# Performance work log

Measured on AMD Instinct MI355X. Metric: run time of the kernel, lower is better.

Reference implementation:

```python
import jax, jax.numpy as jnp
import numpy as np

NEG = -1e9


def _lstm_step(x, h, c, W_ih, W_hh, b_ih, b_hh):
    # torch LSTM gate order: i, f, g, o
    gates = x @ W_ih.T + b_ih + h @ W_hh.T + b_hh
    i, f, g, o = jnp.split(gates, 4, axis=-1)
    c_new = jax.nn.sigmoid(f) * c + jax.nn.sigmoid(i) * jnp.tanh(g)
    h_new = jax.nn.sigmoid(o) * jnp.tanh(c_new)
    return h_new, c_new


def _forward(encoder_states, emb, W_ih, W_hh, b_ih, b_hh, W_att,
             pad_mask, pointer_mask, token_ids, target_sequence,
             sos_token, eos_token, output_len):
    B, N, D = encoder_states.shape
    V = emb.shape[0]
    dt = encoder_states.dtype
    padf = pad_mask.astype(dt)
    enc = encoder_states * padf[..., None]          # zero padded node states
    # _init_lstm_state: mean of encoder states over valid nodes (pad-only mask)
    h0 = enc.sum(axis=1) / padf.sum(axis=1, keepdims=True)  # [B, D]
    # attention mask after pointer restriction: only valid leaf pointer nodes
    attn_mask = jnp.where(pointer_mask, jnp.asarray(0.0, dt), jnp.asarray(NEG, dt))
    n_ptr = pointer_mask.sum(axis=1).astype(dt)     # [B]
    thr = 1.0 / n_ptr                               # _threshold_cf = 1.0
    b_idx = jnp.arange(B)

    # teacher forcing: step 1 uses SOS, step s>1 uses target_sequence[s-1]
    sos_row = jnp.full((1, B), sos_token, dtype=target_sequence.dtype)
    inputs = jnp.concatenate([sos_row, target_sequence[1:output_len - 1]], axis=0)  # [T-1, B]

    def step(carry, inp):
        h, c = carry
        x = emb[inp]                                     # [B, E]
        h, c = _lstm_step(x, h, c, W_ih, W_hh, b_ih, b_hh)
        # Luong attention -> probabilities over tree nodes
        scores = jnp.einsum('bnd,bd->bn', enc, h @ W_att.T) + attn_mask
        probs = jax.nn.softmax(scores, axis=1)           # [B, N]
        # threshold: probabilities below 1/n_ptr are zeroed; only pointer nodes kept
        probs = jnp.where(pointer_mask & (probs >= thr[:, None]), probs, jnp.asarray(0.0, dt))
        # scatter(reduce='sum') node probabilities into vocab-sized output
        out = jnp.zeros((B, V), dt).at[b_idx[:, None], token_ids].add(probs)
        out = out.at[:, eos_token].set(1.0 - probs.sum(axis=1))
        return (h, c), out

    (_, _), outs = jax.lax.scan(step, (h0, h0), inputs)   # [T-1, B, V]
    out0 = jnp.zeros((B, V), dt).at[:, sos_token].set(1.0)
    return jnp.concatenate([out0[None], outs], axis=0)    # [T, B, V]


def setup_inputs() -> dict:
    key = jax.random.key(0)
    ks = jax.random.split(key, 10)
    B, N, D, E, V, T = 32, 2048, 512, 512, 32000, 32
    encoder_states = jax.random.normal(ks[0], (B, N, D), dtype=jnp.float32)
    lengths = jax.random.randint(ks[1], (B,), N // 2, N + 1)
    pad_mask = jnp.arange(N)[None, :] < lengths[:, None]            # [B, N] ragged trees
    leaf = jax.random.bernoulli(ks[2], 0.5, (B, N))
    pointer_mask = pad_mask & leaf                                  # valid leaf pointer nodes
    token_ids = jax.random.randint(ks[3], (B, N), 0, V, dtype=jnp.int32)
    target_sequence = jax.random.randint(ks[4], (T, B), 3, V, dtype=jnp.int32)
    s = 0.02
    emb = jax.random.normal(ks[5], (V, E), dtype=jnp.float32) * s
    W_ih = jax.random.normal(ks[6], (4 * D, E), dtype=jnp.float32) * s
    W_hh = jax.random.normal(ks[7], (4 * D, D), dtype=jnp.float32) * s
    b_ih = jnp.zeros((4 * D,), dtype=jnp.float32)
    b_hh = jnp.zeros((4 * D,), dtype=jnp.float32)
    W_att = jax.random.normal(ks[8], (D, D), dtype=jnp.float32) * s
    return {
        'encoder_states': encoder_states, 'emb': emb,
        'W_ih': W_ih, 'W_hh': W_hh, 'b_ih': b_ih, 'b_hh': b_hh, 'W_att': W_att,
        'pad_mask': pad_mask, 'pointer_mask': pointer_mask,
        'token_ids': token_ids, 'target_sequence': target_sequence,
        'sos_token': 1, 'eos_token': 2, 'output_len': T,
    }


def reference(encoder_states, emb, W_ih, W_hh, b_ih, b_hh, W_att,
              pad_mask, pointer_mask, token_ids, target_sequence,
              sos_token, eos_token, output_len):
    return _forward(encoder_states, emb, W_ih, W_hh, b_ih, b_hh, W_att,
                    pad_mask, pointer_mask, token_ids, target_sequence,
                    sos_token, eos_token, output_len)
```

## Files before the change

### kernel.cpp

```cpp
#include <hip/hip_runtime.h>
#include <math.h>

#define BB 32
#define NN 2048
#define DD 512
#define VV 32000
#define NSTEP 31

__device__ inline float sigm(float x){ return 1.0f/(1.0f+expf(-x)); }
__device__ inline float dot4(float4 a, float4 b){
  return a.x*b.x + a.y*b.y + a.z*b.z + a.w*b.w;
}

__device__ inline float red8(float a0,float a1,float a2,float a3,
                             float a4,float a5,float a6,float a7,int lane){
  float m01 = ((lane&1)? a1:a0) + __shfl_xor(((lane&1)? a0:a1),1,64);
  float m23 = ((lane&1)? a3:a2) + __shfl_xor(((lane&1)? a2:a3),1,64);
  float m45 = ((lane&1)? a5:a4) + __shfl_xor(((lane&1)? a4:a5),1,64);
  float m67 = ((lane&1)? a7:a6) + __shfl_xor(((lane&1)? a6:a7),1,64);
  float m03 = ((lane&2)? m23:m01) + __shfl_xor(((lane&2)? m01:m23),2,64);
  float m47 = ((lane&2)? m67:m45) + __shfl_xor(((lane&2)? m45:m67),2,64);
  float m   = ((lane&4)? m47:m03) + __shfl_xor(((lane&4)? m03:m47),4,64);
  m += __shfl_xor(m,8,64); m += __shfl_xor(m,16,64); m += __shfl_xor(m,32,64);
  return m;
}

__global__ __launch_bounds__(256) void k_cnt(
    const int* __restrict__ pad, const int* __restrict__ pmask,
    const int* __restrict__ sosp,
    float* __restrict__ cntp, float* __restrict__ thr, float* __restrict__ out,
    unsigned int* __restrict__ flags) {
  __shared__ int r1[256], r2[256];
  int b = blockIdx.x, tid = threadIdx.x;
  if (b == 0) {
    if (tid < 256)
      __hip_atomic_store(&flags[tid], 0u, __ATOMIC_RELAXED,
                         __HIP_MEMORY_SCOPE_AGENT);
    if (tid == 0)
      __hip_atomic_store(&flags[256], 0u, __ATOMIC_RELAXED,
                         __HIP_MEMORY_SCOPE_AGENT);
  }
  float4* orow4 = (float4*)(out + (size_t)b*VV);
  float4 z = {0.f,0.f,0.f,0.f};
  for (int i = tid; i < VV/4; i += 256) orow4[i] = z;
  int cp = 0, cq = 0;
  for (int n = tid; n < NN; n += 256) { cp += pad[b*NN+n]; cq += pmask[b*NN+n]; }
  r1[tid] = cp; r2[tid] = cq; __syncthreads();
  for (int st = 128; st; st >>= 1) {
    if (tid < st) { r1[tid] += r1[tid+st]; r2[tid] += r2[tid+st]; }
    __syncthreads();
  }
  if (tid == 0) {
    cntp[b] = (float)r1[0];
    thr[b]  = 1.0f/(float)r2[0];
    out[(size_t)b*VV + sosp[0]] = 1.0f;
  }
}

__global__ __launch_bounds__(128) void k_meanpart(
    const float* __restrict__ enc, const int* __restrict__ pad,
    float* __restrict__ hpart) {
  int b = blockIdx.x, ch = blockIdx.y, kq = threadIdx.x;
  int n0 = ch*32;
  float4 acc = {0.f,0.f,0.f,0.f};
#pragma unroll 8
  for (int r = 0; r < 32; r++) {
    int n = n0 + r;
    float msk = (float)pad[b*NN + n];
    float4 v = *(const float4*)(enc + ((size_t)(b*NN + n))*DD + kq*4);
    acc.x += msk*v.x; acc.y += msk*v.y; acc.z += msk*v.z; acc.w += msk*v.w;
  }
  *(float4*)(hpart + ((size_t)(b*64 + ch))*DD + kq*4) = acc;
}

__global__ __launch_bounds__(128) void k_meanfin(
    const float* __restrict__ hpart, const float* __restrict__ cntp,
    float* __restrict__ h0, float* __restrict__ c) {
  int b = blockIdx.x, kq = threadIdx.x;
  float4 acc = {0.f,0.f,0.f,0.f};
  for (int ch = 0; ch < 64; ch++) {
    float4 v = *(const float4*)(hpart + ((size_t)(b*64 + ch))*DD + kq*4);
    acc.x += v.x; acc.y += v.y; acc.z += v.z; acc.w += v.w;
  }
  float ic = 1.0f/cntp[b];
  acc.x *= ic; acc.y *= ic; acc.z *= ic; acc.w *= ic;
  *(float4*)(h0 + b*DD + kq*4) = acc;
  *(float4*)(c  + b*DD + kq*4) = acc;
}

__global__ __launch_bounds__(512, 2) void k_hloop(
    const float* __restrict__ h0, const float* __restrict__ Whh,
    const float* __restrict__ Wih, const float* __restrict__ bih,
    const float* __restrict__ bhh, const float* __restrict__ emb,
    const int* __restrict__ target, const int* __restrict__ sosp,
    float* __restrict__ H, unsigned int* __restrict__ flags) {
  __shared__ float spad[20736];
  float* g   = spad;
  float* Gls = spad + 256;
  int bi = blockIdx.x, d0 = bi*2;
  int tid = threadIdx.x;
  int w = tid>>6, lane = tid&63;
  float4 W0[8], W1[8], Wi0[8], Wi1[8];
#pragma unroll
  for (int j = 0; j < 8; j++) {
    int r = (j>>1)*DD + d0 + (j&1);
    const float* wp = Whh + (size_t)r*DD + lane*4;
    W0[j]  = *(const float4*)wp; W1[j]  = *(const float4*)(wp + 256);
    const float* ip = Wih + (size_t)r*DD + lane*4;
    Wi0[j] = *(const float4*)ip; Wi1[j] = *(const float4*)(ip + 256);
  }
  int jrole = lane & 7;
  int brow = (jrole>>1)*DD + d0 + (jrole&1);
  float biasj = bih[brow] + bhh[brow];
  int pb = tid>>1, pdd = tid&1;
  float creg = 0.f;
  if (tid < 64) creg = h0[pb*DD + d0 + pdd];

  {
    int sos = sosp[0];
    const float* xp = emb + (size_t)sos*DD + lane*4;
    float4 x0 = *(const float4*)xp, x1 = *(const float4*)(xp + 256);
    float a0 = dot4(x0,Wi0[0]) + dot4(x1,Wi1[0]);
    float a1 = dot4(x0,Wi0[1]) + dot4(x1,Wi1[1]);
    float a2 = dot4(x0,Wi0[2]) + dot4(x1,Wi1[2]);
    float a3 = dot4(x0,Wi0[3]) + dot4(x1,Wi1[3]);
    float a4 = dot4(x0,Wi0[4]) + dot4(x1,Wi1[4]);
    float a5 = dot4(x0,Wi0[5]) + dot4(x1,Wi1[5]);
    float a6 = dot4(x0,Wi0[6]) + dot4(x1,Wi1[6]);
    float a7 = dot4(x0,Wi0[7]) + dot4(x1,Wi1[7]);
    float v = red8(a0,a1,a2,a3,a4,a5,a6,a7,lane);
    if (lane < 8) {
      float vb = v + biasj;
#pragma unroll
      for (int bb = 0; bb < 4; bb++) Gls[(w*4+bb)*8 + lane] = vb;
    }
  }
  __syncthreads();

  for (int s = 0; s < NSTEP; s++) {
#pragma unroll
    for (int j = 0; j < 8; j++) {
      asm volatile("" : "+v"(W0[j].x), "+v"(W0[j].y),
                        "+v"(W0[j].z), "+v"(W0[j].w),
                        "+v"(W1[j].x), "+v"(W1[j].y),
                        "+v"(W1[j].z), "+v"(W1[j].w));
      asm volatile("" : "+v"(Wi0[j].x), "+v"(Wi0[j].y),
                        "+v"(Wi0[j].z), "+v"(Wi0[j].w),
                        "+v"(Wi1[j].x), "+v"(Wi1[j].y),
                        "+v"(Wi1[j].z), "+v"(Wi1[j].w));
    }
    const float* hin = (s == 0) ? h0 : (H + (size_t)(s-1)*BB*DD);
#pragma unroll
    for (int bb = 0; bb < 4; bb++) {
      int b = w*4 + bb;
      const float* hp = hin + b*DD + lane*4;
      float4 h0v = *(const float4*)hp, h1v = *(const float4*)(hp + 256);
      float a0 = dot4(h0v,W0[0]) + dot4(h1v,W1[0]);
      float a1 = dot4(h0v,W0[1]) + dot4(h1v,W1[1]);
      float a2 = dot4(h0v,W0[2]) + dot4(h1v,W1[2]);
      float a3 = dot4(h0v,W0[3]) + dot4(h1v,W1[3]);
      float a4 = dot4(h0v,W0[4]) + dot4(h1v,W1[4]);
      float a5 = dot4(h0v,W0[5]) + dot4(h1v,W1[5]);
      float a6 = dot4(h0v,W0[6]) + dot4(h1v,W1[6]);
      float a7 = dot4(h0v,W0[7]) + dot4(h1v,W1[7]);
      float v = red8(a0,a1,a2,a3,a4,a5,a6,a7,lane);
      if (lane < 8) g[b*8 + lane] = v;
    }
    float4 xg0[4], xg1[4];
    if (s < NSTEP-1) {
#pragma unroll
      for (int bb = 0; bb < 4; bb++) {
        int tg = target[(s+1)*BB + w*4 + bb];
        const float* xp = emb + (size_t)tg*DD + lane*4;
        xg0[bb] = *(const float4*)xp; xg1[bb] = *(const float4*)(xp + 256);
      }
    }
    __syncthreads();
    if (tid < 64) {
      const float* Gs = Gls + (s&1)*256;
      float gi = g[pb*8 + 0 + pdd] + Gs[pb*8 + 0 + pdd];
      float gf = g[pb*8 + 2 + pdd] + Gs[pb*8 + 2 + pdd];
      float gg = g[pb*8 + 4 + pdd] + Gs[pb*8 + 4 + pdd];
      float go = g[pb*8 + 6 + pdd] + Gs[pb*8 + 6 + pdd];
      creg = sigm(gf)*creg + sigm(gi)*tanhf(gg);
      float hn = sigm(go)*tanhf(creg);
      __hip_atomic_store(H + (size_t)s*BB*DD + pb*DD + d0 + pdd, hn,
                         __ATOMIC_RELAXED, __HIP_MEMORY_SCOPE_AGENT);
    }
    if (s == NSTEP-1) break;
    __syncthreads();
    unsigned tgt = (unsigned)(s+1);
    if (tid == 0)
      __hip_atomic_store(&flags[bi], tgt,
                         __ATOMIC_RELAXED, __HIP_MEMORY_SCOPE_AGENT);
    {
      float* Gd = Gls + ((s+1)&1)*256;
#pragma unroll
      for (int bb = 0; bb < 4; bb++) {
        float a0 = dot4(xg0[bb],Wi0[0]) + dot4(xg1[bb],Wi1[0]);
        float a1 = dot4(xg0[bb],Wi0[1]) + dot4(xg1[bb],Wi1[1]);
        float a2 = dot4(xg0[bb],Wi0[2]) + dot4(xg1[bb],Wi1[2]);
        float a3 = dot4(xg0[bb],Wi0[3]) + dot4(xg1[bb],Wi1[3]);
        float a4 = dot4(xg0[bb],Wi0[4]) + dot4(xg1[bb],Wi1[4]);
        float a5 = dot4(xg0[bb],Wi0[5]) + dot4(xg1[bb],Wi1[5]);
        float a6 = dot4(xg0[bb],Wi0[6]) + dot4(xg1[bb],Wi1[6]);
        float a7 = dot4(xg0[bb],Wi0[7]) + dot4(xg1[bb],Wi1[7]);
        float v = red8(a0,a1,a2,a3,a4,a5,a6,a7,lane);
        if (lane < 8) Gd[(w*4+bb)*8 + lane] = v + biasj;
      }
    }
    if (bi == 0 && tid < 64) {
      const unsigned int* fp = flags + tid*4;
      for (;;) {
        unsigned f0 = __hip_atomic_load(fp+0, __ATOMIC_RELAXED,
                                        __HIP_MEMORY_SCOPE_AGENT);
        unsigned f1 = __hip_atomic_load(fp+1, __ATOMIC_RELAXED,
                                        __HIP_MEMORY_SCOPE_AGENT);
        unsigned f2 = __hip_atomic_load(fp+2, __ATOMIC_RELAXED,
                                        __HIP_MEMORY_SCOPE_AGENT);
        unsigned f3 = __hip_atomic_load(fp+3, __ATOMIC_RELAXED,
                                        __HIP_MEMORY_SCOPE_AGENT);
        if (f0 >= tgt && f1 >= tgt && f2 >= tgt && f3 >= tgt) break;
        __builtin_amdgcn_s_sleep(1);
      }
      if (tid == 0)
        __hip_atomic_store(&flags[256], tgt,
                           __ATOMIC_RELAXED, __HIP_MEMORY_SCOPE_AGENT);
    }
    if (tid == 0) {
      while (__hip_atomic_load(&flags[256], __ATOMIC_RELAXED,
                               __HIP_MEMORY_SCOPE_AGENT) < tgt)
        __builtin_amdgcn_s_sleep(1);
    }
    __syncthreads();
  }
}

__global__ __launch_bounds__(256) void k_qallw(
    const float* __restrict__ H, const float* __restrict__ Watt,
    float* __restrict__ Q) {
  int nt = blockIdx.x, mg = blockIdx.y;
  int w = threadIdx.x>>6, lane = threadIdx.x&63;
  int m0 = mg*32 + w*8;
  float4 x0[8], x1[8];
#pragma unroll
  for (int j = 0; j < 8; j++) {
    const float* xp = H + (size_t)(m0 + j)*DD + lane*4;
    x0[j] = *(const float4*)xp; x1[j] = *(const float4*)(xp + 256);
  }
  int r0 = nt*16;
#pragma unroll 2
  for (int i = 0; i < 16; i++) {
    int r = r0 + i;
    const float* wp = Watt + (size_t)r*DD + lane*4;
    float4 w0 = *(const float4*)wp, w1 = *(const float4*)(wp + 256);
    float a0 = dot4(w0,x0[0]) + dot4(w1,x1[0]);
    float a1 = dot4(w0,x0[1]) + dot4(w1,x1[1]);
    float a2 = dot4(w0,x0[2]) + dot4(w1,x1[2]);
    float a3 = dot4(w0,x0[3]) + dot4(w1,x1[3]);
    float a4 = dot4(w0,x0[4]) + dot4(w1,x1[4]);
    float a5 = dot4(w0,x0[5]) + dot4(w1,x1[5]);
    float a6 = dot4(w0,x0[6]) + dot4(w1,x1[6]);
    float a7 = dot4(w0,x0[7]) + dot4(w1,x1[7]);
    float v = red8(a0,a1,a2,a3,a4,a5,a6,a7,lane);
    if (lane < 8) Q[(size_t)(m0 + lane)*DD + r] = v;
  }
}

__global__ __launch_bounds__(256) void k_scores3(
    const float* __restrict__ enc, const float* __restrict__ Q,
    float* __restrict__ S) {
  int nt = blockIdx.x, b = blockIdx.y;
  int w = threadIdx.x>>6, lane = threadIdx.x&63;
  int s0 = w*8;
  float4 q0[8], q1[8];
#pragma unroll
  for (int j = 0; j < 8; j++) {
    const float* qp = Q + (size_t)((s0 + j)*BB + b)*DD + lane*4;
    q0[j] = *(const float4*)qp; q1[j] = *(const float4*)(qp + 256);
  }
  int n0 = nt*32;
  int sl = s0 + (lane & 7);
#pragma unroll 2
  for (int i = 0; i < 32; i++) {
    int n = n0 + i;
    const float* ep = enc + ((size_t)(b*NN + n))*DD + lane*4;
    float4 e0 = *(const float4*)ep, e1 = *(const float4*)(ep + 256);
    float a0 = dot4(e0,q0[0]) + dot4(e1,q1[0]);
    float a1 = dot4(e0,q0[1]) + dot4(e1,q1[1]);
    float a2 = dot4(e0,q0[2]) + dot4(e1,q1[2]);
    float a3 = dot4(e0,q0[3]) + dot4(e1,q1[3]);
    float a4 = dot4(e0,q0[4]) + dot4(e1,q1[4]);
    float a5 = dot4(e0,q0[5]) + dot4(e1,q1[5]);
    float a6 = dot4(e0,q0[6]) + dot4(e1,q1[6]);
    float a7 = dot4(e0,q0[7]) + dot4(e1,q1[7]);
    float v = red8(a0,a1,a2,a3,a4,a5,a6,a7,lane);
    if (lane < 8 && sl < NSTEP) S[((size_t)sl*BB + b)*NN + n] = v;
  }
}

__global__ __launch_bounds__(256) void k_scatter2(
    const float* __restrict__ S, const int* __restrict__ pmask,
    const int* __restrict__ tok, const float* __restrict__ thr,
    const int* __restrict__ eosp, float* __restrict__ out) {
  __shared__ float red[256];
  __shared__ float ex[NN];
  int s = blockIdx.x, b = blockIdx.y, tid = threadIdx.x;
  float* orow = out + ((size_t)(s+1)*BB + b)*VV;
  float4 z = {0.f,0.f,0.f,0.f};
  float4* orow4 = (float4*)orow;
  for (int i = tid; i < VV/4; i += 256) orow4[i] = z;
  const float* sr = S + ((size_t)s*BB + b)*NN;
  const int* pm = pmask + b*NN;
  float m = -3.4e38f;
  for (int n = tid; n < NN; n += 256) if (pm[n]) m = fmaxf(m, sr[n]);
  red[tid] = m; __syncthreads();
  for (int st = 128; st; st >>= 1) {
    if (tid < st) red[tid] = fmaxf(red[tid], red[tid+st]);
    __syncthreads();
  }
  float smax = red[0]; __syncthreads();
  float sum = 0.f;
  for (int n = tid; n < NN; n += 256) {
    float e = pm[n] ? expf(sr[n] - smax) : 0.f;
    ex[n] = e; sum += e;
  }
  red[tid] = sum; __syncthreads();
  for (int st = 128; st; st >>= 1) {
    if (tid < st) red[tid] += red[tid+st];
    __syncthreads();
  }
  float inv = 1.0f/red[0];
  float th = thr[b];
  float keep = 0.f;
  for (int n = tid; n < NN; n += 256) {
    float p = ex[n]*inv;
    if (p >= th) { atomicAdd(orow + tok[b*NN + n], p); keep += p; }
  }
  __syncthreads();
  red[tid] = keep; __syncthreads();
  for (int st = 128; st; st >>= 1) {
    if (tid < st) red[tid] += red[tid+st];
    __syncthreads();
  }
  if (tid == 0) orow[eosp[0]] = 1.0f - red[0];
}

extern "C" void kernel_launch(void* const* d_in, const int* in_sizes, int n_in,
                              void* d_out, int out_size, void* d_ws, size_t ws_size,
                              hipStream_t stream) {
  const float* enc   = (const float*)d_in[0];
  const float* emb   = (const float*)d_in[1];
  const float* Wih   = (const float*)d_in[2];
  const float* Whh   = (const float*)d_in[3];
  const float* bih   = (const float*)d_in[4];
  const float* bhh   = (const float*)d_in[5];
  const float* Watt  = (const float*)d_in[6];
  const int*   pad   = (const int*)d_in[7];
  const int*   pmask = (const int*)d_in[8];
  const int*   tok   = (const int*)d_in[9];
  const int*   target= (const int*)d_in[10];
  const int*   sosp  = (const int*)d_in[11];
  const int*   eosp  = (const int*)d_in[12];
  float* out = (float*)d_out;

  float* w    = (float*)d_ws;
  float* c    = w;
  float* h0   = c    + BB*DD;
  float* H    = h0   + BB*DD;
  float* Q    = H    + NSTEP*BB*DD;
  float* S    = Q    + 32*BB*DD;
  float* G0   = S    + (size_t)NSTEP*BB*NN;
  float* cntp = G0   + (size_t)992*2048;
  float* thr  = cntp + 32;
  unsigned int* flags = (unsigned int*)(thr + 32);
  float* hpart = G0;

  k_cnt<<<32, 256, 0, stream>>>(pad, pmask, sosp, cntp, thr, out, flags);
  k_meanpart<<<dim3(32,64), 128, 0, stream>>>(enc, pad, hpart);
  k_meanfin<<<32, 128, 0, stream>>>(hpart, cntp, h0, c);

  k_hloop<<<256, 512, 0, stream>>>(h0, Whh, Wih, bih, bhh, emb, target, sosp,
                                   H, flags);

  k_qallw<<<dim3(32,31), 256, 0, stream>>>(H, Watt, Q);
  k_scores3<<<dim3(64,32), 256, 0, stream>>>(enc, Q, S);
  k_scatter2<<<dim3(NSTEP,32), 256, 0, stream>>>(S, pmask, tok, thr, eosp, out);
}
```

Before: 602.5 us.

## Fuse attention query projection into recurrent loop and decentralize grid barrier

Each recurrent-loop block now keeps two rows of W_att in registers and computes its slice of Q = h·W_attᵀ for the previous step, overlapping the work with the grid barrier wait. This removes the separate k_qallw launch and its reload of H. The two-level barrier, where block 0 gathers flags and broadcasts a release word, is replaced by every block polling all flags directly with a cache-bypassing vector load and a wave-wide __all. This shortens the barrier critical path but adds polling traffic from 256 blocks and more register pressure.

Measured after the change: 598.7 us. Within noise of the previous version (-0.6%).

```diff
diff --git a/kernel.cpp b/kernel.cpp
--- a/kernel.cpp
+++ b/kernel.cpp
@@ -25,6 +25,14 @@
   return m;
 }
 
+__device__ inline uint4 fresh_load4(const unsigned int* p){
+  uint4 r;
+  asm volatile("global_load_dwordx4 %0, %1, off sc0 sc1\n\t"
+               "s_waitcnt vmcnt(0)"
+               : "=&v"(r) : "v"(p) : "memory");
+  return r;
+}
+
 __global__ __launch_bounds__(256) void k_cnt(
     const int* __restrict__ pad, const int* __restrict__ pmask,
     const int* __restrict__ sosp,
@@ -32,14 +40,9 @@
     unsigned int* __restrict__ flags) {
   __shared__ int r1[256], r2[256];
   int b = blockIdx.x, tid = threadIdx.x;
-  if (b == 0) {
-    if (tid < 256)
-      __hip_atomic_store(&flags[tid], 0u, __ATOMIC_RELAXED,
-                         __HIP_MEMORY_SCOPE_AGENT);
-    if (tid == 0)
-      __hip_atomic_store(&flags[256], 0u, __ATOMIC_RELAXED,
-                         __HIP_MEMORY_SCOPE_AGENT);
-  }
+  if (b == 0 && tid < 256)
+    __hip_atomic_store(&flags[tid], 0u, __ATOMIC_RELAXED,
+                       __HIP_MEMORY_SCOPE_AGENT);
   float4* orow4 = (float4*)(out + (size_t)b*VV);
   float4 z = {0.f,0.f,0.f,0.f};
   for (int i = tid; i < VV/4; i += 256) orow4[i] = z;
@@ -92,15 +95,16 @@
     const float* __restrict__ h0, const float* __restrict__ Whh,
     const float* __restrict__ Wih, const float* __restrict__ bih,
     const float* __restrict__ bhh, const float* __restrict__ emb,
-    const int* __restrict__ target, const int* __restrict__ sosp,
-    float* __restrict__ H, unsigned int* __restrict__ flags) {
+    const float* __restrict__ Watt, const int* __restrict__ target,
+    const int* __restrict__ sosp, float* __restrict__ H,
+    float* __restrict__ Q, unsigned int* __restrict__ flags) {
   __shared__ float spad[20736];
   float* g   = spad;
   float* Gls = spad + 256;
   int bi = blockIdx.x, d0 = bi*2;
   int tid = threadIdx.x;
   int w = tid>>6, lane = tid&63;
-  float4 W0[8], W1[8], Wi0[8], Wi1[8];
+  float4 W0[8], W1[8], Wi0[8], Wi1[8], Wa0[2], Wa1[2];
 #pragma unroll
   for (int j = 0; j < 8; j++) {
     int r = (j>>1)*DD + d0 + (j&1);
@@ -108,6 +112,11 @@
     W0[j]  = *(const float4*)wp; W1[j]  = *(const float4*)(wp + 256);
     const float* ip = Wih + (size_t)r*DD + lane*4;
     Wi0[j] = *(const float4*)ip; Wi1[j] = *(const float4*)(ip + 256);
+  }
+#pragma unroll
+  for (int e = 0; e < 2; e++) {
+    const float* ap = Watt + (size_t)(d0+e)*DD + lane*4;
+    Wa0[e] = *(const float4*)ap; Wa1[e] = *(const float4*)(ap + 256);
   }
   int jrole = lane & 7;
   int brow = (jrole>>1)*DD + d0 + (jrole&1);
@@ -137,6 +146,7 @@
   }
   __syncthreads();
 
+  float4 h0s[4], h1s[4];
   for (int s = 0; s < NSTEP; s++) {
 #pragma unroll
     for (int j = 0; j < 8; j++) {
@@ -149,12 +159,20 @@
                         "+v"(Wi1[j].x), "+v"(Wi1[j].y),
                         "+v"(Wi1[j].z), "+v"(Wi1[j].w));
     }
+#pragma unroll
+    for (int e = 0; e < 2; e++) {
+      asm volatile("" : "+v"(Wa0[e].x), "+v"(Wa0[e].y),
+                        "+v"(Wa0[e].z), "+v"(Wa0[e].w),
+                        "+v"(Wa1[e].x), "+v"(Wa1[e].y),
+                        "+v"(Wa1[e].z), "+v"(Wa1[e].w));
+    }
     const float* hin = (s == 0) ? h0 : (H + (size_t)(s-1)*BB*DD);
 #pragma unroll
     for (int bb = 0; bb < 4; bb++) {
       int b = w*4 + bb;
       const float* hp = hin + b*DD + lane*4;
       float4 h0v = *(const float4*)hp, h1v = *(const float4*)(hp + 256);
+      h0s[bb] = h0v; h1s[bb] = h1v;
       float a0 = dot4(h0v,W0[0]) + dot4(h1v,W1[0]);
       float a1 = dot4(h0v,W0[1]) + dot4(h1v,W1[1]);
       float a2 = dot4(h0v,W0[2]) + dot4(h1v,W1[2]);
@@ -187,13 +205,12 @@
       __hip_atomic_store(H + (size_t)s*BB*DD + pb*DD + d0 + pdd, hn,
                          __ATOMIC_RELAXED, __HIP_MEMORY_SCOPE_AGENT);
     }
-    if (s == NSTEP-1) break;
     __syncthreads();
     unsigned tgt = (unsigned)(s+1);
     if (tid == 0)
       __hip_atomic_store(&flags[bi], tgt,
                          __ATOMIC_RELAXED, __HIP_MEMORY_SCOPE_AGENT);
-    {
+    if (s < NSTEP-1) {
       float* Gd = Gls + ((s+1)&1)*256;
 #pragma unroll
       for (int bb = 0; bb < 4; bb++) {
@@ -209,61 +226,38 @@
         if (lane < 8) Gd[(w*4+bb)*8 + lane] = v + biasj;
       }
     }
-    if (bi == 0 && tid < 64) {
+    if (s > 0) {
+#pragma unroll
+      for (int bb = 0; bb < 4; bb++) {
+        float q0 = dot4(h0s[bb],Wa0[0]) + dot4(h1s[bb],Wa1[0]);
+        float q1 = dot4(h0s[bb],Wa0[1]) + dot4(h1s[bb],Wa1[1]);
+        float v = red8(q0,q1,0.f,0.f,0.f,0.f,0.f,0.f,lane);
+        if (lane < 2)
+          Q[((size_t)(s-1)*BB + w*4 + bb)*DD + d0 + lane] = v;
+      }
+    }
+    if (tid < 64) {
       const unsigned int* fp = flags + tid*4;
       for (;;) {
-        unsigned f0 = __hip_atomic_load(fp+0, __ATOMIC_RELAXED,
-                                        __HIP_MEMORY_SCOPE_AGENT);
-        unsigned f1 = __hip_atomic_load(fp+1, __ATOMIC_RELAXED,
-                                        __HIP_MEMORY_SCOPE_AGENT);
-        unsigned f2 = __hip_atomic_load(fp+2, __ATOMIC_RELAXED,
-                                        __HIP_MEMORY_SCOPE_AGENT);
-        unsigned f3 = __hip_atomic_load(fp+3, __ATOMIC_RELAXED,
-                                        __HIP_MEMORY_SCOPE_AGENT);
-        if (f0 >= tgt && f1 >= tgt && f2 >= tgt && f3 >= tgt) break;
+        uint4 f = fresh_load4(fp);
+        bool ok = f.x >= tgt && f.y >= tgt && f.z >= tgt && f.w >= tgt;
+        if (__all(ok)) break;
         __builtin_amdgcn_s_sleep(1);
       }
-      if (tid == 0)
-        __hip_atomic_store(&flags[256], tgt,
-                           __ATOMIC_RELAXED, __HIP_MEMORY_SCOPE_AGENT);
-    }
-    if (tid == 0) {
-      while (__hip_atomic_load(&flags[256], __ATOMIC_RELAXED,
-                               __HIP_MEMORY_SCOPE_AGENT) < tgt)
-        __builtin_amdgcn_s_sleep(1);
-    }
-    __syncthreads();
-  }
-}
-
-__global__ __launch_bounds__(256) void k_qallw(
-    const float* __restrict__ H, const float* __restrict__ Watt,
-    float* __restrict__ Q) {
-  int nt = blockIdx.x, mg = blockIdx.y;
-  int w = threadIdx.x>>6, lane = threadIdx.x&63;
-  int m0 = mg*32 + w*8;
-  float4 x0[8], x1[8];
-#pragma unroll
-  for (int j = 0; j < 8; j++) {
-    const float* xp = H + (size_t)(m0 + j)*DD + lane*4;
-    x0[j] = *(const float4*)xp; x1[j] = *(const float4*)(xp + 256);
-  }
-  int r0 = nt*16;
-#pragma unroll 2
-  for (int i = 0; i < 16; i++) {
-    int r = r0 + i;
-    const float* wp = Watt + (size_t)r*DD + lane*4;
-    float4 w0 = *(const float4*)wp, w1 = *(const float4*)(wp + 256);
-    float a0 = dot4(w0,x0[0]) + dot4(w1,x1[0]);
-    float a1 = dot4(w0,x0[1]) + dot4(w1,x1[1]);
-    float a2 = dot4(w0,x0[2]) + dot4(w1,x1[2]);
-    float a3 = dot4(w0,x0[3]) + dot4(w1,x1[3]);
-    float a4 = dot4(w0,x0[4]) + dot4(w1,x1[4]);
-    float a5 = dot4(w0,x0[5]) + dot4(w1,x1[5]);
-    float a6 = dot4(w0,x0[6]) + dot4(w1,x1[6]);
-    float a7 = dot4(w0,x0[7]) + dot4(w1,x1[7]);
-    float v = red8(a0,a1,a2,a3,a4,a5,a6,a7,lane);
-    if (lane < 8) Q[(size_t)(m0 + lane)*DD + r] = v;
+    }
+    __syncthreads();
+  }
+
+#pragma unroll
+  for (int bb = 0; bb < 4; bb++) {
+    int b = w*4 + bb;
+    const float* hp = H + (size_t)(NSTEP-1)*BB*DD + b*DD + lane*4;
+    float4 h0v = *(const float4*)hp, h1v = *(const float4*)(hp + 256);
+    float q0 = dot4(h0v,Wa0[0]) + dot4(h1v,Wa1[0]);
+    float q1 = dot4(h0v,Wa0[1]) + dot4(h1v,Wa1[1]);
+    float v = red8(q0,q1,0.f,0.f,0.f,0.f,0.f,0.f,lane);
+    if (lane < 2)
+      Q[((size_t)(NSTEP-1)*BB + b)*DD + d0 + lane] = v;
   }
 }
 
@@ -380,10 +374,9 @@
   k_meanpart<<<dim3(32,64), 128, 0, stream>>>(enc, pad, hpart);
   k_meanfin<<<32, 128, 0, stream>>>(hpart, cntp, h0, c);
 
-  k_hloop<<<256, 512, 0, stream>>>(h0, Whh, Wih, bih, bhh, emb, target, sosp,
-                                   H, flags);
-
-  k_qallw<<<dim3(32,31), 256, 0, stream>>>(H, Watt, Q);
+  k_hloop<<<256, 512, 0, stream>>>(h0, Whh, Wih, bih, bhh, emb, Watt, target,
+                                   sosp, H, Q, flags);
+
   k_scores3<<<dim3(64,32), 256, 0, stream>>>(enc, Q, S);
   k_scatter2<<<dim3(NSTEP,32), 256, 0, stream>>>(S, pmask, tok, thr, eosp, out);
 }
```
